# Kernel tuning notes

Measured on AMD Instinct MI355X. Metric: run time of the kernel, lower is better.

## Reference

```python
import jax, jax.numpy as jnp
import numpy as np

N = 4096          # total ensemble boxes per frame
M = 20            # MAX_MERGE_NUMS
H = 16            # MergeNet hidden_c
COND_THRES = 0.2
IOU_THRES = 0.3


def setup_inputs() -> dict:
    key = jax.random.key(0)
    ks = jax.random.split(key, 6)
    u = jax.random.uniform(ks[0], (N, 9), dtype=jnp.float32)
    # realistic lidar boxes: centers in a ~140x80x8m range, dims in [0.5, 4.5), heading in [-pi, pi)
    centers = (u[:, 0:3] - 0.5) * jnp.array([140.0, 80.0, 8.0], jnp.float32)
    dims = u[:, 3:6] * 4.0 + 0.5
    heading = (u[:, 6:7] - 0.5) * (2.0 * np.pi)
    extra = u[:, 7:9]  # extra box attrs (cols 7:9), untouched by merge
    pred_boxes = jnp.concatenate([centers, dims, heading, extra], axis=-1)
    pred_scores = jax.random.uniform(ks[1], (N,), dtype=jnp.float32)
    pred_labels = jax.random.randint(ks[2], (N,), 0, 3)
    w1 = (jax.random.normal(ks[3], (M, H), jnp.float32) / np.sqrt(M)).astype(jnp.float32)
    b1 = jnp.zeros((H,), jnp.float32)
    w2 = (jax.random.normal(ks[4], (H, H), jnp.float32) / np.sqrt(H)).astype(jnp.float32)
    b2 = jnp.zeros((H,), jnp.float32)
    w3 = (jax.random.normal(ks[5], (H, 1), jnp.float32) / np.sqrt(H)).astype(jnp.float32)
    b3 = jnp.zeros((1,), jnp.float32)
    return dict(pred_boxes=pred_boxes, pred_scores=pred_scores, pred_labels=pred_labels,
                w1=w1, b1=b1, w2=w2, b2=b2, w3=w3, b3=b3)


def _bev_aligned(b):
    # boxes3d_lidar_to_aligned_bev_boxes: swap dx/dy when |limit_period(heading)| >= pi/4
    ang = b[..., 6] - jnp.floor(b[..., 6] / np.pi + 0.5) * np.pi
    swap = jnp.abs(ang) >= (np.pi / 4)
    dx = jnp.where(swap, b[..., 4], b[..., 3])
    dy = jnp.where(swap, b[..., 3], b[..., 4])
    return jnp.stack([b[..., 0] - dx / 2, b[..., 1] - dy / 2,
                      b[..., 0] + dx / 2, b[..., 1] + dy / 2], axis=-1)


def _iou_one_many(a, b):
    # axis-aligned BEV IoU of one box a[4] vs many b[N,4]
    xmin = jnp.maximum(a[0], b[:, 0]); ymin = jnp.maximum(a[1], b[:, 1])
    xmax = jnp.minimum(a[2], b[:, 2]); ymax = jnp.minimum(a[3], b[:, 3])
    inter = jnp.maximum(xmax - xmin, 0.0) * jnp.maximum(ymax - ymin, 0.0)
    area_a = (a[2] - a[0]) * (a[3] - a[1])
    area_b = (b[:, 2] - b[:, 0]) * (b[:, 3] - b[:, 1])
    return inter / jnp.maximum(area_a + area_b - inter, 1e-6)


def _nms_merge(pred_boxes, pred_scores, pred_labels, w1, b1, w2, b2, w3, b3):
    valid = pred_scores > COND_THRES
    sort_key = jnp.where(valid, pred_scores, -jnp.inf)
    order = jnp.argsort(-sort_key)                 # descending by score; invalid sink
    boxes9 = pred_boxes[order]
    labels = pred_labels[order]
    scores = pred_scores[order]
    suppressed0 = ~valid[order]
    boxes7 = boxes9[:, :7]
    bev0 = _bev_aligned(boxes7)                    # merged boxes get suppressed, so bev is static

    def mergenet(ob):                              # ob: [M, 7] -> merged box [7]
        x = ob.T                                   # [7, M] (k is the feature axis)
        h = jax.nn.relu(x @ w1 + b1)
        h = jax.nn.relu(h @ w2 + b2)
        return (h @ w3 + b3)[:, 0]

    def step(suppressed, i):
        active = ~suppressed[i]
        same = (labels == labels[i]) & (~suppressed)
        iou = _iou_one_many(bev0[i], bev0)         # [N]
        over = (iou > IOU_THRES) & same            # includes self (iou=1)
        count = jnp.sum(over)
        rank = jnp.cumsum(over) - 1                # slot of each overlap, in score order
        tgt = jnp.where(over & (rank < M), rank, M)
        ob = jnp.zeros((M, 7), boxes7.dtype).at[tgt].set(boxes7, mode='drop')
        bi = boxes7[i]
        new_box = jnp.where(count > 1, mergenet(ob), bi)
        new_box = new_box.at[3:6].set(jnp.maximum(new_box[3:6], 1e-5))
        out_box = jnp.where(active, new_box, bi)
        return suppressed | (over & active), (out_box, active)

    _, (merged7, keep) = jax.lax.scan(step, suppressed0, jnp.arange(N))
    out_boxes = jnp.concatenate([merged7, boxes9[:, 7:9]], axis=-1)   # [N, 9]
    return out_boxes, scores, labels, keep


def reference(pred_boxes, pred_scores, pred_labels, w1, b1, w2, b2, w3, b3):
    # Returns fixed-shape (boxes9, scores, labels, keep_mask); rows with keep=False
    # correspond to boxes that torch's dynamic version would have removed.
    return _nms_merge(pred_boxes, pred_scores, pred_labels, w1, b1, w2, b2, w3, b3)
```

## Files before the change

### kernel.cpp

```cpp
#include <hip/hip_runtime.h>
#include <cstdint>

typedef unsigned long long u64;
typedef unsigned int u32;

#define NB 4096
#define NW 64
#define MM 20
#define HH 16
#define COND_THRES 0.2f
#define IOU_THRES 0.3f
#define PI_F  3.14159265358979323846f
#define PI4_F 0.78539816339744830962f

#define WS_KEPT    0
#define WS_MASK    32768
#define WS_BOX9S   (WS_MASK + NB*NW*8)
#define WS_BEVS    (WS_BOX9S + NB*9*4)
#define WS_SCORES  (WS_BEVS + NB*16)
#define WS_LABELS  (WS_SCORES + NB*4)
#define WS_NBRW    (WS_LABELS + NB*4)

__device__ __forceinline__ u64 sort_key(float s, int i) {
  u32 sb = (s > COND_THRES) ? __float_as_uint(s) : 0u;
  return ((u64)(sb ^ 0xFFFFFFFFu) << 12) | (u64)i;
}

__global__ void __launch_bounds__(256) k_prep(const float* __restrict__ scores,
                                              const float* __restrict__ boxes9,
                                              const int* __restrict__ labels,
                                              float* __restrict__ box9s, float4* __restrict__ bevs,
                                              float* __restrict__ scoress, int* __restrict__ labelss,
                                              u64* __restrict__ nbrw) {
  #pragma clang fp contract(off)
  __shared__ u64 keys[NB];
  __shared__ u32 part[16][16];
  int tid = threadIdx.x;
  for (int k = tid; k < NB; k += 256) keys[k] = sort_key(scores[k], k);
  __syncthreads();
  int bl = tid & 15;
  int ch = tid >> 4;
  u64 ki = keys[blockIdx.x * 16 + bl];
  int c = 0;
  #pragma unroll 16
  for (int t = 0; t < 256; ++t) c += (keys[(ch << 8) + t] < ki) ? 1 : 0;
  part[bl][ch] = (u32)c;
  __syncthreads();
  if (tid < 16) {
    int i = blockIdx.x * 16 + tid;
    int r = 0;
    #pragma unroll
    for (int q = 0; q < 16; ++q) r += (int)part[tid][q];
    nbrw[i] = 0;
    float b[9];
    #pragma unroll
    for (int f = 0; f < 9; ++f) b[f] = boxes9[i * 9 + f];
    #pragma unroll
    for (int f = 0; f < 9; ++f) box9s[r * 9 + f] = b[f];
    float ang = b[6] - floorf(b[6] / PI_F + 0.5f) * PI_F;
    bool sw = fabsf(ang) >= PI4_F;
    float dx = sw ? b[4] : b[3];
    float dy = sw ? b[3] : b[4];
    bevs[r] = make_float4(b[0] - dx * 0.5f, b[1] - dy * 0.5f,
                          b[0] + dx * 0.5f, b[1] + dy * 0.5f);
    scoress[r] = scores[i];
    labelss[r] = labels[i];
  }
}

__global__ void __launch_bounds__(64) k_mask(const float4* __restrict__ bevs,
                                             const int* __restrict__ labelss,
                                             const float* __restrict__ scoress,
                                             u64* __restrict__ mask,
                                             u64* __restrict__ nbrw) {
  #pragma clang fp contract(off)
  __shared__ float4 bj[64];
  __shared__ int lj[64];
  __shared__ u64 tw[64];
  int t = threadIdx.x;
  int jt = blockIdx.x;
  int it = blockIdx.y;
  if (jt > it) return;
  int j = jt * 64 + t;
  bj[t] = bevs[j];
  lj[t] = labelss[j];
  u64 vj = __ballot(scoress[j] > COND_THRES);
  int i = it * 64 + t;
  float4 a = bevs[i];
  int la = labelss[i];
  float area_a = (a.z - a.x) * (a.w - a.y);
  __syncthreads();
  u64 w = 0;
  #pragma unroll 8
  for (int kk = 0; kk < 64; ++kk) {
    float4 bb = bj[kk];
    float xmin = fmaxf(a.x, bb.x), ymin = fmaxf(a.y, bb.y);
    float xmax = fminf(a.z, bb.z), ymax = fminf(a.w, bb.w);
    float inter = fmaxf(xmax - xmin, 0.0f) * fmaxf(ymax - ymin, 0.0f);
    float area_b = (bb.z - bb.x) * (bb.w - bb.y);
    float iou = inter / fmaxf(area_a + area_b - inter, 1e-6f);
    if ((iou > IOU_THRES) && (la == lj[kk])) w |= (1ull << kk);
  }
  mask[(u64)i * NW + jt] = w;
  {
    u64 below = (jt < it) ? ~0ull : ((1ull << t) - 1ull);
    if (w & vj & below) atomicOr(&nbrw[i], 1ull << jt);
  }
  if (jt < it) {
    tw[t] = w;
    __syncthreads();
    u64 wT = 0;
    #pragma unroll 8
    for (int k = 0; k < 64; ++k) wT |= ((tw[k] >> t) & 1ull) << k;
    mask[(u64)j * NW + it] = wT;
  }
}

__global__ void __launch_bounds__(1024) k_nms(const u64* __restrict__ mask,
                                              const u64* __restrict__ nbrw,
                                              const float* __restrict__ scoress,
                                              u64* __restrict__ keptOut) {
  __shared__ u64 decided[64], kept[64];
  __shared__ int wavePending[16];
  __shared__ int anyPending;
  int tid = threadIdx.x;
  int lane = tid & 63;
  int waveId = tid >> 6;
  u64 dcache[4], kcache[4];
  #pragma unroll
  for (int s = 0; s < 4; ++s) {
    int i = tid + (s << 10);
    bool v = scoress[i] > COND_THRES;
    u64 vw = __ballot(v);
    dcache[s] = ~vw;
    kcache[s] = 0;
    if (lane == 0) {
      int wi = waveId + (s << 4);
      decided[wi] = ~vw;
      kept[wi] = 0;
    }
  }
  u64 cw0[4], cw1[4];
  u32 meta[4];
  #pragma unroll
  for (int s = 0; s < 4; ++s) {
    int i = tid + (s << 10);
    int wi = i >> 6;
    u64 bit = 1ull << (i & 63);
    u64 t = nbrw[i];
    int n = 0; u32 ovf = 0;
    u64 c0 = 0, c1 = 0; u32 i0 = 0, i1 = 0;
    while (t) {
      int w = __builtin_ctzll(t);
      t &= t - 1;
      u64 below = (w < wi) ? ~0ull : (bit - 1ull);
      u64 m = mask[(u64)i * NW + w] & below;
      if (n == 0)      { c0 = m; i0 = (u32)w; }
      else if (n == 1) { c1 = m; i1 = (u32)w; }
      else ovf = 1;
      ++n;
    }
    cw0[s] = c0; cw1[s] = c1;
    meta[s] = i0 | (i1 << 6) | ((u32)(n > 2 ? 2 : n) << 12) | (ovf << 14);
  }
  __syncthreads();
  while (true) {
    bool pend = false;
    #pragma unroll
    for (int s = 0; s < 4; ++s) {
      bool mine_und = !((dcache[s] >> lane) & 1ull);
      bool dec = false, keepme = false;
      if (mine_und) {
        bool hasU = false, hasK = false;
        u32 mt = meta[s];
        if (!(mt & (1u << 14))) {
          int n = (mt >> 12) & 3;
          if (n >= 1) {
            int w = mt & 63;
            u64 dw = decided[w], kw = kept[w];
            hasU = (cw0[s] & ~dw) != 0ull;
            hasK = (cw0[s] & kw) != 0ull;
          }
          if (n >= 2) {
            int w = (mt >> 6) & 63;
            u64 dw = decided[w], kw = kept[w];
            hasU = hasU || ((cw1[s] & ~dw) != 0ull);
            hasK = hasK || ((cw1[s] & kw) != 0ull);
          }
        } else {
          int i = tid + (s << 10);
          int wi = i >> 6;
          u64 bit = 1ull << (i & 63);
          u64 t = nbrw[i];
          while (t) {
            int w = __builtin_ctzll(t);
            t &= t - 1;
            u64 below = (w < wi) ? ~0ull : (bit - 1ull);
            u64 m = mask[(u64)i * NW + w] & below;
            hasU = hasU || ((m & ~decided[w]) != 0ull);
            hasK = hasK || ((m & kept[w]) != 0ull);
          }
        }
        dec = !hasU;
        keepme = !hasK;
      }
      u64 b_nd = __ballot(dec);
      u64 b_nk = __ballot(dec && keepme);
      dcache[s] |= b_nd;
      kcache[s] |= b_nk;
      pend |= (mine_und && !dec);
    }
    u64 pw = __ballot(pend);
    if (lane == 0) wavePending[waveId] = (pw != 0ull) ? 1 : 0;
    __syncthreads();
    if (lane == 0) {
      #pragma unroll
      for (int s = 0; s < 4; ++s) {
        int wi = waveId + (s << 4);
        decided[wi] = dcache[s];
        kept[wi] = kcache[s];
      }
    }
    if (tid == 0) {
      int any = 0;
      #pragma unroll
      for (int w = 0; w < 16; ++w) any |= wavePending[w];
      anyPending = any;
    }
    __syncthreads();
    if (!anyPending) break;
  }
  if (tid < 64) keptOut[tid] = kept[tid];
}

__global__ void __launch_bounds__(64) k_merge(
    const u64* __restrict__ mask, const u64* __restrict__ keptG,
    const float* __restrict__ box9s, const float* __restrict__ scoress,
    const int* __restrict__ labelss,
    const float* __restrict__ w1, const float* __restrict__ b1,
    const float* __restrict__ w2, const float* __restrict__ b2,
    const float* __restrict__ w3, const float* __restrict__ b3,
    float* __restrict__ out) {
  #pragma clang fp contract(off)
  __shared__ int candList[MM];
  __shared__ float ob[MM][7];
  __shared__ float h1[7][HH];
  __shared__ float h2[7][HH];
  __shared__ float res[7];
  __shared__ u64 K[64];
  int i = blockIdx.x;
  int t = threadIdx.x;
  K[t] = keptG[t];
  __syncthreads();
  bool active = (K[i >> 6] >> (i & 63)) & 1ull;
  u64 wq = 0;
  int cnt = 0;
  if (active) {
    u64 w = mask[(u64)i * NW + t];
    int hiw = i >> 6;
    u64 below = (1ull << (i & 63)) - 1ull;
    while (w) {
      int b = __builtin_ctzll(w);
      w &= w - 1;
      int j = (t << 6) | b;
      if (scoress[j] > COND_THRES) {
        const u64* rowj = mask + (u64)j * NW;
        u64 found = rowj[hiw] & K[hiw] & below;
        for (int ww = 0; ww < hiw; ++ww) found |= rowj[ww] & K[ww];
        if (!found) { wq |= (1ull << b); cnt++; }
      }
    }
  }
  int incl = cnt;
  #pragma unroll
  for (int off = 1; off < 64; off <<= 1) {
    int v = __shfl_up(incl, off);
    if (t >= off) incl += v;
  }
  int excl = incl - cnt;
  int count = __shfl(incl, 63);
  bool merged = active && (count > 1);
  if (merged && wq) {
    int pos = excl;
    u64 ww = wq;
    while (ww && pos < MM) {
      int b = __builtin_ctzll(ww);
      ww &= ww - 1;
      candList[pos++] = (t << 6) | b;
    }
  }
  __syncthreads();
  if (merged) {
    int nc = count < MM ? count : MM;
    if (t < MM) {
      if (t < nc) {
        int j = candList[t];
        #pragma unroll
        for (int f = 0; f < 7; ++f) ob[t][f] = box9s[j * 9 + f];
      } else {
        #pragma unroll
        for (int f = 0; f < 7; ++f) ob[t][f] = 0.0f;
      }
    }
    __syncthreads();
    for (int o = t; o < 7 * HH; o += 64) {
      int f = o >> 4, hh = o & 15;
      float acc = b1[hh];
      #pragma unroll
      for (int m = 0; m < MM; ++m) acc += ob[m][f] * w1[m * HH + hh];
      h1[f][hh] = fmaxf(acc, 0.0f);
    }
    __syncthreads();
    for (int o = t; o < 7 * HH; o += 64) {
      int f = o >> 4, oo = o & 15;
      float acc = b2[oo];
      #pragma unroll
      for (int k = 0; k < HH; ++k) acc += h1[f][k] * w2[k * HH + oo];
      h2[f][oo] = fmaxf(acc, 0.0f);
    }
    __syncthreads();
    if (t < 7) {
      float acc = b3[0];
      #pragma unroll
      for (int k = 0; k < HH; ++k) acc += h2[t][k] * w3[k];
      if (t >= 3 && t < 6) acc = fmaxf(acc, 1e-5f);
      res[t] = acc;
    }
    __syncthreads();
  }
  if (t < 9) {
    float v = box9s[i * 9 + t];
    if (merged && t < 7) v = res[t];
    out[i * 9 + t] = v;
  }
  if (t == 0) {
    out[NB * 9 + i]          = scoress[i];
    out[NB * 9 + NB + i]     = (float)labelss[i];
    out[NB * 9 + 2 * NB + i] = active ? 1.0f : 0.0f;
  }
}

extern "C" void kernel_launch(void* const* d_in, const int* in_sizes, int n_in,
                              void* d_out, int out_size, void* d_ws, size_t ws_size,
                              hipStream_t stream) {
  const float* boxes9 = (const float*)d_in[0];
  const float* scores = (const float*)d_in[1];
  const int*   labels = (const int*)d_in[2];
  const float* w1 = (const float*)d_in[3];
  const float* b1 = (const float*)d_in[4];
  const float* w2 = (const float*)d_in[5];
  const float* b2 = (const float*)d_in[6];
  const float* w3 = (const float*)d_in[7];
  const float* b3 = (const float*)d_in[8];
  char* ws = (char*)d_ws;
  u64*    kept    = (u64*)(ws + WS_KEPT);
  u64*    mask    = (u64*)(ws + WS_MASK);
  float*  box9s   = (float*)(ws + WS_BOX9S);
  float4* bevs    = (float4*)(ws + WS_BEVS);
  float*  scoress = (float*)(ws + WS_SCORES);
  int*    labelss = (int*)(ws + WS_LABELS);
  u64*    nbrw    = (u64*)(ws + WS_NBRW);
  float*  out     = (float*)d_out;

  hipLaunchKernelGGL(k_prep,  dim3(256),    dim3(256),  0, stream,
                     scores, boxes9, labels, box9s, bevs, scoress, labelss, nbrw);
  hipLaunchKernelGGL(k_mask,  dim3(64, 64), dim3(64),   0, stream,
                     bevs, labelss, scoress, mask, nbrw);
  hipLaunchKernelGGL(k_nms,   dim3(1),      dim3(1024), 0, stream,
                     mask, nbrw, scoress, kept);
  hipLaunchKernelGGL(k_merge, dim3(NB),     dim3(64),   0, stream,
                     mask, kept, box9s, scoress, labelss,
                     w1, b1, w2, b2, w3, b3, out);
}
```

Baseline: 119.6 us.

## Precompute per-box suppression step in NMS; launch only lower-triangular mask tiles

The NMS kernel now records, for each valid box, the index of the first kept box that suppresses it (itself if kept) by scanning its neighbour words. The merge kernel uses this value to decide which overlaps were still unsuppressed at step i, replacing a per-candidate loop over up to 64 mask words. Separately, the mask kernel launches 2080 blocks covering only the lower triangle instead of a 64x64 grid where half the blocks exit early. The new pass adds serial work to the single-block NMS kernel and an extra workspace buffer.

```diff
diff --git a/kernel.cpp b/kernel.cpp
--- a/kernel.cpp
+++ b/kernel.cpp
@@ -20,6 +20,7 @@
 #define WS_SCORES  (WS_BEVS + NB*16)
 #define WS_LABELS  (WS_SCORES + NB*4)
 #define WS_NBRW    (WS_LABELS + NB*4)
+#define WS_SUPSTEP (WS_NBRW + NB*8)
 
 __device__ __forceinline__ u64 sort_key(float s, int i) {
   u32 sb = (s > COND_THRES) ? __float_as_uint(s) : 0u;
@@ -78,9 +79,11 @@
   __shared__ int lj[64];
   __shared__ u64 tw[64];
   int t = threadIdx.x;
-  int jt = blockIdx.x;
-  int it = blockIdx.y;
-  if (jt > it) return;
+  int b = blockIdx.x;
+  int it = (int)((sqrtf(8.0f * (float)b + 1.0f) - 1.0f) * 0.5f);
+  while ((it + 1) * (it + 2) / 2 <= b) ++it;
+  while (it * (it + 1) / 2 > b) --it;
+  int jt = b - it * (it + 1) / 2;
   int j = jt * 64 + t;
   bj[t] = bevs[j];
   lj[t] = labelss[j];
@@ -119,7 +122,7 @@
 __global__ void __launch_bounds__(1024) k_nms(const u64* __restrict__ mask,
                                               const u64* __restrict__ nbrw,
                                               const float* __restrict__ scoress,
-                                              u64* __restrict__ keptOut) {
+                                              int* __restrict__ supstep) {
   __shared__ u64 decided[64], kept[64];
   __shared__ int wavePending[16];
   __shared__ int anyPending;
@@ -127,10 +130,12 @@
   int lane = tid & 63;
   int waveId = tid >> 6;
   u64 dcache[4], kcache[4];
+  bool validB[4];
   #pragma unroll
   for (int s = 0; s < 4; ++s) {
     int i = tid + (s << 10);
     bool v = scoress[i] > COND_THRES;
+    validB[s] = v;
     u64 vw = __ballot(v);
     dcache[s] = ~vw;
     kcache[s] = 0;
@@ -230,11 +235,31 @@
     __syncthreads();
     if (!anyPending) break;
   }
-  if (tid < 64) keptOut[tid] = kept[tid];
+  #pragma unroll
+  for (int s = 0; s < 4; ++s) {
+    int j = tid + (s << 10);
+    int res;
+    if (!validB[s]) {
+      res = -1;
+    } else {
+      int wj = j >> 6;
+      u64 bitbelow = (1ull << (j & 63)) - 1ull;
+      res = j;
+      u64 t = nbrw[j];
+      while (t) {
+        int w = __builtin_ctzll(t);
+        t &= t - 1;
+        u64 m = mask[(u64)j * NW + w] & kept[w];
+        if (w == wj) m &= bitbelow;
+        if (m) { res = (w << 6) + __builtin_ctzll(m); break; }
+      }
+    }
+    supstep[j] = res;
+  }
 }
 
 __global__ void __launch_bounds__(64) k_merge(
-    const u64* __restrict__ mask, const u64* __restrict__ keptG,
+    const u64* __restrict__ mask, const int* __restrict__ supstep,
     const float* __restrict__ box9s, const float* __restrict__ scoress,
     const int* __restrict__ labelss,
     const float* __restrict__ w1, const float* __restrict__ b1,
@@ -247,28 +272,18 @@
   __shared__ float h1[7][HH];
   __shared__ float h2[7][HH];
   __shared__ float res[7];
-  __shared__ u64 K[64];
   int i = blockIdx.x;
   int t = threadIdx.x;
-  K[t] = keptG[t];
-  __syncthreads();
-  bool active = (K[i >> 6] >> (i & 63)) & 1ull;
+  bool active = (supstep[i] == i);
   u64 wq = 0;
   int cnt = 0;
   if (active) {
     u64 w = mask[(u64)i * NW + t];
-    int hiw = i >> 6;
-    u64 below = (1ull << (i & 63)) - 1ull;
     while (w) {
       int b = __builtin_ctzll(w);
       w &= w - 1;
       int j = (t << 6) | b;
-      if (scoress[j] > COND_THRES) {
-        const u64* rowj = mask + (u64)j * NW;
-        u64 found = rowj[hiw] & K[hiw] & below;
-        for (int ww = 0; ww < hiw; ++ww) found |= rowj[ww] & K[ww];
-        if (!found) { wq |= (1ull << b); cnt++; }
-      }
+      if (supstep[j] >= i) { wq |= (1ull << b); cnt++; }
     }
   }
   int incl = cnt;
@@ -353,22 +368,22 @@
   const float* w3 = (const float*)d_in[7];
   const float* b3 = (const float*)d_in[8];
   char* ws = (char*)d_ws;
-  u64*    kept    = (u64*)(ws + WS_KEPT);
   u64*    mask    = (u64*)(ws + WS_MASK);
   float*  box9s   = (float*)(ws + WS_BOX9S);
   float4* bevs    = (float4*)(ws + WS_BEVS);
   float*  scoress = (float*)(ws + WS_SCORES);
   int*    labelss = (int*)(ws + WS_LABELS);
   u64*    nbrw    = (u64*)(ws + WS_NBRW);
+  int*    supstep = (int*)(ws + WS_SUPSTEP);
   float*  out     = (float*)d_out;
 
-  hipLaunchKernelGGL(k_prep,  dim3(256),    dim3(256),  0, stream,
+  hipLaunchKernelGGL(k_prep,  dim3(256),  dim3(256),  0, stream,
                      scores, boxes9, labels, box9s, bevs, scoress, labelss, nbrw);
-  hipLaunchKernelGGL(k_mask,  dim3(64, 64), dim3(64),   0, stream,
+  hipLaunchKernelGGL(k_mask,  dim3(2080), dim3(64),   0, stream,
                      bevs, labelss, scoress, mask, nbrw);
-  hipLaunchKernelGGL(k_nms,   dim3(1),      dim3(1024), 0, stream,
-                     mask, nbrw, scoress, kept);
-  hipLaunchKernelGGL(k_merge, dim3(NB),     dim3(64),   0, stream,
-                     mask, kept, box9s, scoress, labelss,
+  hipLaunchKernelGGL(k_nms,   dim3(1),    dim3(1024), 0, stream,
+                     mask, nbrw, scoress, supstep);
+  hipLaunchKernelGGL(k_merge, dim3(NB),   dim3(64),   0, stream,
+                     mask, supstep, box9s, scoress, labelss,
                      w1, b1, w2, b2, w3, b3, out);
 }
```

Result: faster. 112.8 us (-5.6%).
